# Kernel optimization log

Measured on AMD Instinct MI355X. Metric: run time of the kernel, lower is better.

## Reference

```python
import jax, jax.numpy as jnp
import numpy as np

HIDDEN = 2048
NUM_HEADS = 16
HEAD_DIM = HIDDEN // NUM_HEADS
HARMONICS = 64


def _holo_params(key, in_features, out_features, harmonics):
    kb, kp = jax.random.split(key)
    basis = jax.random.normal(kb, (harmonics, in_features), dtype=jnp.float32)
    basis = basis / jnp.linalg.norm(basis, axis=1, keepdims=True)  # F.normalize(p=2, dim=1)
    phase = jax.random.normal(kp, (out_features, harmonics), dtype=jnp.float32) * 0.1
    amp = jnp.ones((out_features, harmonics), dtype=jnp.float32) / np.sqrt(harmonics).astype(np.float32)
    return basis, phase, amp


def setup_inputs() -> dict:
    key = jax.random.key(0)
    ks = jax.random.split(key, 5)
    hidden_states = jax.random.normal(ks[0], (2, 2048, HIDDEN), dtype=jnp.float32)
    inp = {"hidden_states": hidden_states}
    for name, k in zip(("q", "k", "v", "o"), ks[1:]):
        basis, phase, amp = _holo_params(k, HIDDEN, HIDDEN, HARMONICS)
        inp[f"basis_{name}"] = basis
        inp[f"phase_{name}"] = phase
        inp[f"amp_{name}"] = amp
    return inp


def _holo_linear(x, basis, phase, amp):
    # resonance: (B,S,H) = x @ basis^T; modulated-sum == resonance @ (amp*cos(phase))^T
    resonance = jnp.einsum('bsd,hd->bsh', x, basis)
    w = amp * jnp.cos(phase)  # (out, harmonics)
    return jnp.einsum('bsh,oh->bso', resonance, w)


def reference(hidden_states, basis_q, phase_q, amp_q, basis_k, phase_k, amp_k,
              basis_v, phase_v, amp_v, basis_o, phase_o, amp_o):
    bsz, seq_len, _ = hidden_states.shape
    q = _holo_linear(hidden_states, basis_q, phase_q, amp_q)
    k = _holo_linear(hidden_states, basis_k, phase_k, amp_k)
    v = _holo_linear(hidden_states, basis_v, phase_v, amp_v)
    # (B, H, S, Dh)
    q = q.reshape(bsz, seq_len, NUM_HEADS, HEAD_DIM).transpose(0, 2, 1, 3)
    k = k.reshape(bsz, seq_len, NUM_HEADS, HEAD_DIM).transpose(0, 2, 1, 3)
    v = v.reshape(bsz, seq_len, NUM_HEADS, HEAD_DIM).transpose(0, 2, 1, 3)
    scale = 1.0 / np.sqrt(HEAD_DIM).astype(np.float32)
    scores = jnp.einsum('bhqd,bhkd->bhqk', q, k) * scale
    attn = jax.nn.softmax(scores, axis=-1)
    out = jnp.einsum('bhqk,bhkd->bhqd', attn, v)
    out = out.transpose(0, 2, 1, 3).reshape(bsz, seq_len, HIDDEN)
    return _holo_linear(out, basis_o, phase_o, amp_o)
```

## Files before the change

kernel.cpp:

```cpp
#include <hip/hip_runtime.h>
#include <hip/hip_bf16.h>
#include <math.h>

#define HIDDEN 2048
#define HARM   64
#define NHEADS 16
#define HDIM   128
#define SEQ    2048
#define BATCH  2
#define ROWS   (BATCH*SEQ)
#define RN     (ROWS*HARM)
#define PN     ((size_t)ROWS*HIDDEN)

using bf16x8 = __attribute__((ext_vector_type(8))) short;
using f32x16 = __attribute__((ext_vector_type(16))) float;

#if defined(__has_builtin)
#if __has_builtin(__builtin_amdgcn_exp2f)
#define EXP2F(x) __builtin_amdgcn_exp2f(x)
#else
#define EXP2F(x) exp2f(x)
#endif
#else
#define EXP2F(x) exp2f(x)
#endif

__device__ inline void split_bf(float a, ushort& hi, ushort& lo) {
  __hip_bfloat16 h = __float2bfloat16(a);
  float hf = __bfloat162float(h);
  __hip_bfloat16 l = __float2bfloat16(a - hf);
  union { __hip_bfloat16 b; ushort u; } c1, c2;
  c1.b = h; c2.b = l;
  hi = c1.u; lo = c2.u;
}

__global__ __launch_bounds__(256) void prep(
    const float* __restrict__ X,
    const float* __restrict__ pq, const float* __restrict__ aq,
    const float* __restrict__ pk, const float* __restrict__ ak,
    const float* __restrict__ pv, const float* __restrict__ av,
    const float* __restrict__ po, const float* __restrict__ ao,
    const float* __restrict__ bq, const float* __restrict__ bk,
    const float* __restrict__ bv, const float* __restrict__ bo,
    ushort* __restrict__ Xh, ushort* __restrict__ Xl,
    ushort* __restrict__ Wh, ushort* __restrict__ Wl,
    ushort* __restrict__ Bh, ushort* __restrict__ Bl) {
  const int bid = blockIdx.x;
  const int t = threadIdx.x;
  if (bid < 8192) {
    size_t i = ((size_t)bid * 256 + t) * 4;
    float4 v = *(const float4*)&X[i];
    ushort4 h, l;
    split_bf(v.x, h.x, l.x); split_bf(v.y, h.y, l.y);
    split_bf(v.z, h.z, l.z); split_bf(v.w, h.w, l.w);
    *(ushort4*)&Xh[i] = h;
    *(ushort4*)&Xl[i] = l;
  } else if (bid < 10240) {
    int i = (bid - 8192) * 256 + t;
    const int N = HIDDEN * HARM;
    int set = i / N, j = i - set * N;
    const float* p = (set == 0) ? pq : (set == 1) ? pk : (set == 2) ? pv : po;
    const float* a = (set == 0) ? aq : (set == 1) ? ak : (set == 2) ? av : ao;
    float wv = a[j] * cosf(p[j]);
    ushort h, l;
    split_bf(wv, h, l);
    size_t o = (size_t)set * N + j;
    Wh[o] = h; Wl[o] = l;
  } else {
    int idx = bid - 10240;
    int z = idx >> 7, xb = idx & 127;
    const float* S = (z == 0) ? bq : (z == 1) ? bk : (z == 2) ? bv : bo;
    size_t i = ((size_t)xb * 256 + t) * 4;
    float4 v = *(const float4*)&S[i];
    ushort4 h, l;
    split_bf(v.x, h.x, l.x); split_bf(v.y, h.y, l.y);
    split_bf(v.z, h.z, l.z); split_bf(v.w, h.w, l.w);
    size_t o = (size_t)z * HARM * HIDDEN + i;
    *(ushort4*)&Bh[o] = h;
    *(ushort4*)&Bl[o] = l;
  }
}

__global__ __launch_bounds__(256) void gemm_res(
    const ushort* __restrict__ Xh, const ushort* __restrict__ Xl,
    const ushort* __restrict__ Bh, const ushort* __restrict__ Bl,
    float* __restrict__ R0, float* __restrict__ R1, float* __restrict__ R2) {
  const int z = blockIdx.z;
  const ushort* Bhz = Bh + (size_t)z * HARM * HIDDEN;
  const ushort* Blz = Bl + (size_t)z * HARM * HIDDEN;
  float* Rp = (z == 0) ? R0 : (z == 1) ? R1 : R2;
  const int row0 = blockIdx.x * 64;
  const int kc = blockIdx.y;
  __shared__ __align__(16) ushort Xs[2][64][72];
  __shared__ __align__(16) ushort Bs[2][64][72];
  const int t = threadIdx.x;
  const int lane = t & 63, w = t >> 6;
  const int l31 = lane & 31, hh = lane >> 5;
  const int m0 = (w & 1) * 32, n0 = (w >> 1) * 32;
  const int srow = t >> 2;
  const int sc = (t & 3) * 16;
  f32x16 acc;
  #pragma unroll
  for (int j = 0; j < 16; ++j) acc[j] = 0.0f;

  const int kbase = kc * 512;
  for (int k0 = kbase; k0 < kbase + 512; k0 += 64) {
    const size_t xo = (size_t)(row0 + srow) * HIDDEN + k0 + sc;
    const size_t bo = (size_t)srow * HIDDEN + k0 + sc;
    *(uint4*)&Xs[0][srow][sc]     = *(const uint4*)&Xh[xo];
    *(uint4*)&Xs[0][srow][sc + 8] = *(const uint4*)&Xh[xo + 8];
    *(uint4*)&Xs[1][srow][sc]     = *(const uint4*)&Xl[xo];
    *(uint4*)&Xs[1][srow][sc + 8] = *(const uint4*)&Xl[xo + 8];
    *(uint4*)&Bs[0][srow][sc]     = *(const uint4*)&Bhz[bo];
    *(uint4*)&Bs[0][srow][sc + 8] = *(const uint4*)&Bhz[bo + 8];
    *(uint4*)&Bs[1][srow][sc]     = *(const uint4*)&Blz[bo];
    *(uint4*)&Bs[1][srow][sc + 8] = *(const uint4*)&Blz[bo + 8];
    __syncthreads();
    #pragma unroll
    for (int ks = 0; ks < 4; ++ks) {
      bf16x8 ah = *(const bf16x8*)&Xs[0][m0 + l31][ks * 16 + 8 * hh];
      bf16x8 al = *(const bf16x8*)&Xs[1][m0 + l31][ks * 16 + 8 * hh];
      bf16x8 bh = *(const bf16x8*)&Bs[0][n0 + l31][ks * 16 + 8 * hh];
      bf16x8 bl = *(const bf16x8*)&Bs[1][n0 + l31][ks * 16 + 8 * hh];
      acc = __builtin_amdgcn_mfma_f32_32x32x16_bf16(ah, bh, acc, 0, 0, 0);
      acc = __builtin_amdgcn_mfma_f32_32x32x16_bf16(al, bh, acc, 0, 0, 0);
      acc = __builtin_amdgcn_mfma_f32_32x32x16_bf16(ah, bl, acc, 0, 0, 0);
    }
    __syncthreads();
  }
  float* out = Rp + (size_t)kc * ROWS * HARM;
  #pragma unroll
  for (int r = 0; r < 16; ++r) {
    int mloc = (r & 3) + 8 * (r >> 2) + 4 * hh;
    out[(size_t)(row0 + m0 + mloc) * HARM + n0 + l31] = acc[r];
  }
}

__global__ __launch_bounds__(256) void gemm_proj(
    const float* __restrict__ Rp0, const float* __restrict__ Rp1,
    const float* __restrict__ Rp2,
    const ushort* __restrict__ Wh, const ushort* __restrict__ Wl,
    ushort* __restrict__ P0, ushort* __restrict__ P1, ushort* __restrict__ Vt) {
  const int z = blockIdx.z;
  const float* Rp = (z == 0) ? Rp0 : (z == 1) ? Rp1 : Rp2;
  const ushort* Whz = Wh + (size_t)z * HIDDEN * HARM;
  const ushort* Wlz = Wl + (size_t)z * HIDDEN * HARM;
  const int row0 = blockIdx.x * 32;
  const int col0 = blockIdx.y * 128;
  __shared__ __align__(16) union PSM {
    struct { ushort Rs[2][32][72]; ushort Ws[2][128][72]; } s;
    ushort ct[128][36];
  } sm;
  const int t = threadIdx.x;
  const int lane = t & 63, w = t >> 6;
  const int l31 = lane & 31, hh = lane >> 5;
  {
    const int r = t >> 3, h0 = (t & 7) * 8;
    const size_t o = (size_t)(row0 + r) * HARM + h0;
    #pragma unroll
    for (int e = 0; e < 8; ++e) {
      float v = Rp[o + e] + Rp[RN + o + e] + Rp[2 * (size_t)RN + o + e] +
                Rp[3 * (size_t)RN + o + e];
      ushort hi, lo;
      split_bf(v, hi, lo);
      sm.s.Rs[0][r][h0 + e] = hi;
      sm.s.Rs[1][r][h0 + e] = lo;
    }
  }
  #pragma unroll
  for (int i = 0; i < 4; ++i) {
    int idx = t + i * 256;
    int o = idx >> 3, c8 = (idx & 7) * 8;
    const size_t go = (size_t)(col0 + o) * HARM + c8;
    *(uint4*)&sm.s.Ws[0][o][c8] = *(const uint4*)&Whz[go];
    *(uint4*)&sm.s.Ws[1][o][c8] = *(const uint4*)&Wlz[go];
  }
  __syncthreads();
  const int n0 = w * 32;
  f32x16 acc;
  #pragma unroll
  for (int j = 0; j < 16; ++j) acc[j] = 0.0f;
  #pragma unroll
  for (int ks = 0; ks < 4; ++ks) {
    bf16x8 ah = *(const bf16x8*)&sm.s.Rs[0][l31][ks * 16 + 8 * hh];
    bf16x8 al = *(const bf16x8*)&sm.s.Rs[1][l31][ks * 16 + 8 * hh];
    bf16x8 bh = *(const bf16x8*)&sm.s.Ws[0][n0 + l31][ks * 16 + 8 * hh];
    bf16x8 bl = *(const bf16x8*)&sm.s.Ws[1][n0 + l31][ks * 16 + 8 * hh];
    acc = __builtin_amdgcn_mfma_f32_32x32x16_bf16(ah, bh, acc, 0, 0, 0);
    acc = __builtin_amdgcn_mfma_f32_32x32x16_bf16(al, bh, acc, 0, 0, 0);
    acc = __builtin_amdgcn_mfma_f32_32x32x16_bf16(ah, bl, acc, 0, 0, 0);
  }
  if (z < 2) {
    ushort* P = (z == 0) ? P0 : P1;
    #pragma unroll
    for (int r = 0; r < 16; ++r) {
      int mloc = (r & 3) + 8 * (r >> 2) + 4 * hh;
      union { __hip_bfloat16 b; ushort u; } cv;
      cv.b = __float2bfloat16(acc[r]);
      P[(size_t)(row0 + mloc) * HIDDEN + col0 + n0 + l31] = cv.u;
    }
  } else {
    __syncthreads();
    #pragma unroll
    for (int r = 0; r < 16; ++r) {
      int mloc = (r & 3) + 8 * (r >> 2) + 4 * hh;
      union { __hip_bfloat16 b; ushort u; } cv;
      cv.b = __float2bfloat16(acc[r]);
      sm.ct[n0 + l31][mloc] = cv.u;
    }
    __syncthreads();
    if (t < 128) {
      const int batch = row0 >> 11;
      const int tok0 = row0 & 2047;
      ushort* dst = Vt + (size_t)batch * SEQ * HIDDEN +
                    (size_t)(col0 + t) * SEQ + tok0;
      #pragma unroll
      for (int j = 0; j < 4; ++j)
        *(uint4*)&dst[j * 8] = *(const uint4*)&sm.ct[t][j * 8];
    }
  }
}

__global__ __launch_bounds__(256) void gemm_proj_f32(
    const float* __restrict__ Rp,
    const ushort* __restrict__ Whz, const ushort* __restrict__ Wlz,
    float* __restrict__ P) {
  const int row0 = blockIdx.x * 32;
  const int col0 = blockIdx.y * 128;
  __shared__ __align__(16) ushort Rs[2][32][72];
  __shared__ __align__(16) ushort Ws[2][128][72];
  const int t = threadIdx.x;
  const int lane = t & 63, w = t >> 6;
  const int l31 = lane & 31, hh = lane >> 5;
  {
    const int r = t >> 3, h0 = (t & 7) * 8;
    const size_t o = (size_t)(row0 + r) * HARM + h0;
    #pragma unroll
    for (int e = 0; e < 8; ++e) {
      float v = Rp[o + e] + Rp[RN + o + e] + Rp[2 * (size_t)RN + o + e] +
                Rp[3 * (size_t)RN + o + e];
      ushort hi, lo;
      split_bf(v, hi, lo);
      Rs[0][r][h0 + e] = hi;
      Rs[1][r][h0 + e] = lo;
    }
  }
  #pragma unroll
  for (int i = 0; i < 4; ++i) {
    int idx = t + i * 256;
    int o = idx >> 3, c8 = (idx & 7) * 8;
    const size_t go = (size_t)(col0 + o) * HARM + c8;
    *(uint4*)&Ws[0][o][c8] = *(const uint4*)&Whz[go];
    *(uint4*)&Ws[1][o][c8] = *(const uint4*)&Wlz[go];
  }
  __syncthreads();
  const int n0 = w * 32;
  f32x16 acc;
  #pragma unroll
  for (int j = 0; j < 16; ++j) acc[j] = 0.0f;
  #pragma unroll
  for (int ks = 0; ks < 4; ++ks) {
    bf16x8 ah = *(const bf16x8*)&Rs[0][l31][ks * 16 + 8 * hh];
    bf16x8 al = *(const bf16x8*)&Rs[1][l31][ks * 16 + 8 * hh];
    bf16x8 bh = *(const bf16x8*)&Ws[0][n0 + l31][ks * 16 + 8 * hh];
    bf16x8 bl = *(const bf16x8*)&Ws[1][n0 + l31][ks * 16 + 8 * hh];
    acc = __builtin_amdgcn_mfma_f32_32x32x16_bf16(ah, bh, acc, 0, 0, 0);
    acc = __builtin_amdgcn_mfma_f32_32x32x16_bf16(al, bh, acc, 0, 0, 0);
    acc = __builtin_amdgcn_mfma_f32_32x32x16_bf16(ah, bl, acc, 0, 0, 0);
  }
  #pragma unroll
  for (int r = 0; r < 16; ++r) {
    int mloc = (r & 3) + 8 * (r >> 2) + 4 * hh;
    P[(size_t)(row0 + mloc) * HIDDEN + col0 + n0 + l31] = acc[r];
  }
}

#define BQ 128
#define BK 64
#define KSTR 136
#define VSTR 72

__device__ inline unsigned pkbf(float a, float b) {
  __hip_bfloat162 h2 = __float22bfloat162_rn(make_float2(a, b));
  union { __hip_bfloat162 h; unsigned u; } cv; cv.h = h2; return cv.u;
}

__global__ __launch_bounds__(256, 2) void attn_mfma(
    const ushort* __restrict__ Qg, const ushort* __restrict__ Kg,
    const ushort* __restrict__ Vt, ushort* __restrict__ Oh,
    ushort* __restrict__ Ol) {
  __shared__ __align__(16) union SM {
    ushort q[BQ][KSTR];
    struct { ushort k[BK][KSTR]; ushort v[HDIM][VSTR]; } kv[2];
  } sm;
  const int t = threadIdx.x;
  const int bh = blockIdx.x & 31;
  const int qt = blockIdx.x >> 5;
  const int b = bh >> 4, h = bh & 15;
  const int q0 = qt * BQ;
  const int lane = t & 63;
  const int w = t >> 6;
  const int l31 = lane & 31;
  const int hh = lane >> 5;
  const bool hi = (hh != 0);
  const float SC2 = 0.08838834764831845f * 1.4426950408889634f;

  const int sk_key = t >> 4;
  const int sk_d0 = (t & 15) * 8;
  const int sv_d = t >> 3;
  const int sv_k = (t & 7) * 8;
  const size_t kbase = ((size_t)(b * SEQ)) * HIDDEN + h * HDIM;
  const size_t vbase = ((size_t)(b * SEQ + h * HDIM)) * SEQ;

  {
    const size_t gbase = ((size_t)(b * SEQ + q0)) * HIDDEN + h * HDIM;
    for (int p = 0; p < 8; ++p) {
      int row = p * 16 + sk_key;
      uint4 v = *(const uint4*)&Qg[gbase + (size_t)row * HIDDEN + sk_d0];
      *(uint4*)&sm.q[row][sk_d0] = v;
    }
  }
  __syncthreads();
  bf16x8 Qf[8];
  {
    const int qrow = w * 32 + l31;
    #pragma unroll
    for (int ks = 0; ks < 8; ++ks)
      Qf[ks] = *(const bf16x8*)&sm.q[qrow][ks * 16 + 8 * hh];
  }
  __syncthreads();

  float mrow = -1e30f, lsum = 0.0f;
  f32x16 Ot[4];
  #pragma unroll
  for (int i = 0; i < 4; ++i)
    #pragma unroll
    for (int j = 0; j < 16; ++j) Ot[i][j] = 0.0f;
  f32x16 Zv;
  #pragma unroll
  for (int j = 0; j < 16; ++j) Zv[j] = 0.0f;

  uint4 kp[4], vp[4];
  {
    const size_t gb = kbase;
    #pragma unroll
    for (int p = 0; p < 4; ++p)
      kp[p] = *(const uint4*)&Kg[gb + (size_t)(p * 16 + sk_key) * HIDDEN + sk_d0];
    #pragma unroll
    for (int p = 0; p < 4; ++p)
      vp[p] = *(const uint4*)&Vt[vbase + (size_t)(p * 32 + sv_d) * SEQ + sv_k];
    #pragma unroll
    for (int p = 0; p < 4; ++p)
      *(uint4*)&sm.kv[0].k[p * 16 + sk_key][sk_d0] = kp[p];
    #pragma unroll
    for (int p = 0; p < 4; ++p)
      *(uint4*)&sm.kv[0].v[p * 32 + sv_d][sv_k] = vp[p];
  }
  __syncthreads();

  for (int ci = 0; ci < 32; ++ci) {
    {
      const int cn = (ci < 31) ? ci + 1 : 31;
      const size_t gb = kbase + (size_t)(cn * BK) * HIDDEN;
      #pragma unroll
      for (int p = 0; p < 4; ++p)
        kp[p] = *(const uint4*)&Kg[gb + (size_t)(p * 16 + sk_key) * HIDDEN + sk_d0];
      const size_t vb = vbase + cn * BK;
      #pragma unroll
      for (int p = 0; p < 4; ++p)
        vp[p] = *(const uint4*)&Vt[vb + (size_t)(p * 32 + sv_d) * SEQ + sv_k];
    }
    const int cb = ci & 1;

    f32x16 C0, C1;
    {
      bf16x8 a0 = *(const bf16x8*)&sm.kv[cb].k[l31][8 * hh];
      bf16x8 a1 = *(const bf16x8*)&sm.kv[cb].k[32 + l31][8 * hh];
      __builtin_amdgcn_s_setprio(1);
      C0 = __builtin_amdgcn_mfma_f32_32x32x16_bf16(a0, Qf[0], Zv, 0, 0, 0);
      C1 = __builtin_amdgcn_mfma_f32_32x32x16_bf16(a1, Qf[0], Zv, 0, 0, 0);
      #pragma unroll
      for (int ks = 1; ks < 8; ++ks) {
        bf16x8 b0 = *(const bf16x8*)&sm.kv[cb].k[l31][ks * 16 + 8 * hh];
        bf16x8 b1 = *(const bf16x8*)&sm.kv[cb].k[32 + l31][ks * 16 + 8 * hh];
        C0 = __builtin_amdgcn_mfma_f32_32x32x16_bf16(b0, Qf[ks], C0, 0, 0, 0);
        C1 = __builtin_amdgcn_mfma_f32_32x32x16_bf16(b1, Qf[ks], C1, 0, 0, 0);
      }
      __builtin_amdgcn_s_setprio(0);
    }

    float m01[16];
    #pragma unroll
    for (int j = 0; j < 16; ++j) m01[j] = fmaxf(C0[j], C1[j]);
    float x0 = fmaxf(fmaxf(m01[0], m01[1]), m01[2]);
    float x1 = fmaxf(fmaxf(m01[3], m01[4]), m01[5]);
    float x2 = fmaxf(fmaxf(m01[6], m01[7]), m01[8]);
    float x3 = fmaxf(fmaxf(m01[9], m01[10]), m01[11]);
    float x4 = fmaxf(fmaxf(m01[12], m01[13]), m01[14]);
    float mxr = fmaxf(fmaxf(fmaxf(x0, x1), fmaxf(x2, x3)), fmaxf(x4, m01[15]));
    mxr = fmaxf(mxr, __shfl_xor(mxr, 32));

    const float mg = mxr * SC2;
    if (__any(mg > mrow)) {
      const float mnew = fmaxf(mrow, mg);
      const float alpha = EXP2F(mrow - mnew);
      lsum *= alpha;
      #pragma unroll
      for (int i = 0; i < 4; ++i)
        #pragma unroll
        for (int j = 0; j < 16; ++j) Ot[i][j] *= alpha;
      mrow = mnew;
    }
    float s0 = 0.0f, s1 = 0.0f, s2 = 0.0f, s3 = 0.0f;
    #pragma unroll
    for (int j = 0; j < 16; ++j) {
      float e0 = EXP2F(fmaf(C0[j], SC2, -mrow));
      float e1 = EXP2F(fmaf(C1[j], SC2, -mrow));
      C0[j] = e0; C1[j] = e1;
      if (j & 1) { s2 += e0; s3 += e1; } else { s0 += e0; s1 += e1; }
    }
    lsum += (s0 + s1) + (s2 + s3);

    #pragma unroll
    for (int st = 0; st < 4; ++st) {
      const int eb = 8 * (st & 1);
      float o0, o1, o2, o3, g0, g1, g2, g3;
      if (st < 2) {
        o0 = hi ? C0[eb + 4] : C0[eb + 0]; o1 = hi ? C0[eb + 5] : C0[eb + 1];
        o2 = hi ? C0[eb + 6] : C0[eb + 2]; o3 = hi ? C0[eb + 7] : C0[eb + 3];
        g0 = hi ? C0[eb + 0] : C0[eb + 4]; g1 = hi ? C0[eb + 1] : C0[eb + 5];
        g2 = hi ? C0[eb + 2] : C0[eb + 6]; g3 = hi ? C0[eb + 3] : C0[eb + 7];
      } else {
        o0 = hi ? C1[eb + 4] : C1[eb + 0]; o1 = hi ? C1[eb + 5] : C1[eb + 1];
        o2 = hi ? C1[eb + 6] : C1[eb + 2]; o3 = hi ? C1[eb + 7] : C1[eb + 3];
        g0 = hi ? C1[eb + 0] : C1[eb + 4]; g1 = hi ? C1[eb + 1] : C1[eb + 5];
        g2 = hi ? C1[eb + 2] : C1[eb + 6]; g3 = hi ? C1[eb + 3] : C1[eb + 7];
      }
      unsigned so0 = pkbf(o0, o1), so1 = pkbf(o2, o3);
      unsigned sp0 = pkbf(g0, g1), sp1 = pkbf(g2, g3);
      unsigned r0 = (unsigned)__shfl_xor((int)sp0, 32);
      unsigned r1 = (unsigned)__shfl_xor((int)sp1, 32);
      union { unsigned u[4]; bf16x8 v; } cv;
      cv.u[0] = hi ? r0 : so0;
      cv.u[1] = hi ? r1 : so1;
      cv.u[2] = hi ? so0 : r0;
      cv.u[3] = hi ? so1 : r1;
      __builtin_amdgcn_s_setprio(1);
      #pragma unroll
      for (int mt = 0; mt < 4; ++mt) {
        bf16x8 a2 = *(const bf16x8*)&sm.kv[cb].v[mt * 32 + l31][st * 16 + 8 * hh];
        Ot[mt] = __builtin_amdgcn_mfma_f32_32x32x16_bf16(a2, cv.v, Ot[mt], 0, 0, 0);
      }
      __builtin_amdgcn_s_setprio(0);
    }

    {
      const int nb = cb ^ 1;
      #pragma unroll
      for (int p = 0; p < 4; ++p)
        *(uint4*)&sm.kv[nb].k[p * 16 + sk_key][sk_d0] = kp[p];
      #pragma unroll
      for (int p = 0; p < 4; ++p)
        *(uint4*)&sm.kv[nb].v[p * 32 + sv_d][sv_k] = vp[p];
    }
    __syncthreads();
  }

  lsum += __shfl_xor(lsum, 32);
  const float inv = 1.0f / lsum;
  const int qrow = q0 + w * 32 + l31;
  const size_t ob = ((size_t)(b * SEQ + qrow)) * HIDDEN + h * HDIM;
  #pragma unroll
  for (int mt = 0; mt < 4; ++mt)
    #pragma unroll
    for (int g = 0; g < 4; ++g) {
      ushort4 hs, ls;
      split_bf(Ot[mt][4 * g + 0] * inv, hs.x, ls.x);
      split_bf(Ot[mt][4 * g + 1] * inv, hs.y, ls.y);
      split_bf(Ot[mt][4 * g + 2] * inv, hs.z, ls.z);
      split_bf(Ot[mt][4 * g + 3] * inv, hs.w, ls.w);
      const size_t off = ob + mt * 32 + 8 * g + 4 * hh;
      *(ushort4*)&Oh[off] = hs;
      *(ushort4*)&Ol[off] = ls;
    }
}

extern "C" void kernel_launch(void* const* d_in, const int* in_sizes, int n_in,
                              void* d_out, int out_size, void* d_ws, size_t ws_size,
                              hipStream_t stream) {
  (void)in_sizes; (void)n_in; (void)out_size; (void)ws_size;
  const float* X       = (const float*)d_in[0];
  const float* basis_q = (const float*)d_in[1];
  const float* phase_q = (const float*)d_in[2];
  const float* amp_q   = (const float*)d_in[3];
  const float* basis_k = (const float*)d_in[4];
  const float* phase_k = (const float*)d_in[5];
  const float* amp_k   = (const float*)d_in[6];
  const float* basis_v = (const float*)d_in[7];
  const float* phase_v = (const float*)d_in[8];
  const float* amp_v   = (const float*)d_in[9];
  const float* basis_o = (const float*)d_in[10];
  const float* phase_o = (const float*)d_in[11];
  const float* amp_o   = (const float*)d_in[12];

  const size_t WN = (size_t)HIDDEN * HARM;

  char* p = (char*)d_ws;
  ushort* Xhi = (ushort*)p; p += PN * 2;
  ushort* Xlo = (ushort*)p; p += PN * 2;
  ushort* Bhi = (ushort*)p; p += 4 * WN * 2;
  ushort* Blo = (ushort*)p; p += 4 * WN * 2;
  ushort* Whi = (ushort*)p; p += 4 * WN * 2;
  ushort* Wlo = (ushort*)p; p += 4 * WN * 2;
  float* Rqp = (float*)p; p += (size_t)4 * RN * 4;
  float* Rkp = (float*)p; p += (size_t)4 * RN * 4;
  float* Rvp = (float*)p; p += (size_t)4 * RN * 4;
  float* Rop = (float*)p; p += (size_t)4 * RN * 4;
  __hip_bfloat16* Qb = (__hip_bfloat16*)p; p += PN * 2;
  __hip_bfloat16* Kb = (__hip_bfloat16*)p; p += PN * 2;
  __hip_bfloat16* VtB = (__hip_bfloat16*)p; p += PN * 2;
  ushort* AOh = (ushort*)p; p += PN * 2;
  ushort* AOl = (ushort*)p; p += PN * 2;
  float* out = (float*)d_out;

  prep<<<10752, 256, 0, stream>>>(X,
                                  phase_q, amp_q, phase_k, amp_k,
                                  phase_v, amp_v, phase_o, amp_o,
                                  basis_q, basis_k, basis_v, basis_o,
                                  Xhi, Xlo, Whi, Wlo, Bhi, Blo);

  gemm_res<<<dim3(64, 4, 3), 256, 0, stream>>>(Xhi, Xlo, Bhi, Blo, Rqp, Rkp, Rvp);

  gemm_proj<<<dim3(128, 16, 3), 256, 0, stream>>>(
      Rqp, Rkp, Rvp, Whi, Wlo, (ushort*)Qb, (ushort*)Kb, (ushort*)VtB);

  attn_mfma<<<dim3((SEQ / BQ) * 32), 256, 0, stream>>>(
      (const ushort*)Qb, (const ushort*)Kb, (const ushort*)VtB, AOh, AOl);

  gemm_res<<<dim3(64, 4, 1), 256, 0, stream>>>(
      AOh, AOl, Bhi + 3 * WN, Blo + 3 * WN, Rop, Rop, Rop);

  gemm_proj_f32<<<dim3(128, 16), 256, 0, stream>>>(
      Rop, Whi + 3 * WN, Wlo + 3 * WN, out);
}
```

Baseline: 257.0 us.

## Fuse Q/K/V resonance GEMMs into one block sharing X tiles; use permlane32 swap

```diff
diff --git a/kernel.cpp b/kernel.cpp
--- a/kernel.cpp
+++ b/kernel.cpp
@@ -14,6 +14,7 @@
 
 using bf16x8 = __attribute__((ext_vector_type(8))) short;
 using f32x16 = __attribute__((ext_vector_type(16))) float;
+using u32x2  = __attribute__((ext_vector_type(2))) unsigned;
 
 #if defined(__has_builtin)
 #if __has_builtin(__builtin_amdgcn_exp2f)
@@ -23,6 +24,37 @@
 #endif
 #else
 #define EXP2F(x) exp2f(x)
+#endif
+
+#if defined(__has_builtin) && __has_builtin(__builtin_amdgcn_permlane32_swap)
+__device__ inline void plane_swap_u(unsigned& a, unsigned& b) {
+  u32x2 r = __builtin_amdgcn_permlane32_swap(a, b, false, false);
+  a = r[0]; b = r[1];
+}
+__device__ inline void plane_swap_f(float& a, float& b) {
+  union { float f; unsigned u; } ua, ub;
+  ua.f = a; ub.f = b;
+  u32x2 r = __builtin_amdgcn_permlane32_swap(ua.u, ub.u, false, false);
+  ua.u = r[0]; ub.u = r[1];
+  a = ua.f; b = ub.f;
+}
+#else
+__device__ inline void plane_swap_u(unsigned& a, unsigned& b) {
+  const bool hi = (threadIdx.x & 32) != 0;
+  unsigned ax = (unsigned)__shfl_xor((int)a, 32);
+  unsigned bx = (unsigned)__shfl_xor((int)b, 32);
+  unsigned r0 = hi ? bx : a;
+  unsigned r1 = hi ? b : ax;
+  a = r0; b = r1;
+}
+__device__ inline void plane_swap_f(float& a, float& b) {
+  const bool hi = (threadIdx.x & 32) != 0;
+  float ax = __shfl_xor(a, 32);
+  float bx = __shfl_xor(b, 32);
+  float r0 = hi ? bx : a;
+  float r1 = hi ? b : ax;
+  a = r0; b = r1;
+}
 #endif
 
 __device__ inline void split_bf(float a, ushort& hi, ushort& lo) {
@@ -81,6 +113,66 @@
   }
 }
 
+__global__ __launch_bounds__(768) void gemm_res3(
+    const ushort* __restrict__ Xh, const ushort* __restrict__ Xl,
+    const ushort* __restrict__ Bh, const ushort* __restrict__ Bl,
+    float* __restrict__ R0, float* __restrict__ R1, float* __restrict__ R2) {
+  const int row0 = blockIdx.x * 64;
+  const int kc = blockIdx.y;
+  __shared__ __align__(16) ushort Xs[2][64][72];
+  __shared__ __align__(16) ushort Bs[3][2][64][72];
+  const int t = threadIdx.x;
+  const int lane = t & 63, w = t >> 6;
+  const int l31 = lane & 31, hh = lane >> 5;
+  const int z = w >> 2;
+  const int wq = w & 3;
+  const int m0 = (wq & 1) * 32, n0 = (wq >> 1) * 32;
+  f32x16 acc;
+  #pragma unroll
+  for (int j = 0; j < 16; ++j) acc[j] = 0.0f;
+
+  const int kbase = kc * 512;
+  for (int k0 = kbase; k0 < kbase + 512; k0 += 64) {
+    #pragma unroll
+    for (int it = 0; it < 6; ++it) {
+      int idx = t + it * 768;
+      if (idx < 4096) {
+        int s = idx >> 9, r = (idx >> 3) & 63, c8 = (idx & 7) * 8;
+        if (s < 2) {
+          const ushort* src = s ? Xl : Xh;
+          *(uint4*)&Xs[s][r][c8] =
+              *(const uint4*)&src[(size_t)(row0 + r) * HIDDEN + k0 + c8];
+        } else {
+          int zz = (s - 2) >> 1, pl = (s - 2) & 1;
+          const ushort* src = pl ? Bl : Bh;
+          *(uint4*)&Bs[zz][pl][r][c8] =
+              *(const uint4*)&src[(size_t)zz * HARM * HIDDEN +
+                                  (size_t)r * HIDDEN + k0 + c8];
+        }
+      }
+    }
+    __syncthreads();
+    #pragma unroll
+    for (int ks = 0; ks < 4; ++ks) {
+      bf16x8 ah = *(const bf16x8*)&Xs[0][m0 + l31][ks * 16 + 8 * hh];
+      bf16x8 al = *(const bf16x8*)&Xs[1][m0 + l31][ks * 16 + 8 * hh];
+      bf16x8 bh = *(const bf16x8*)&Bs[z][0][n0 + l31][ks * 16 + 8 * hh];
+      bf16x8 bl = *(const bf16x8*)&Bs[z][1][n0 + l31][ks * 16 + 8 * hh];
+      acc = __builtin_amdgcn_mfma_f32_32x32x16_bf16(ah, bh, acc, 0, 0, 0);
+      acc = __builtin_amdgcn_mfma_f32_32x32x16_bf16(al, bh, acc, 0, 0, 0);
+      acc = __builtin_amdgcn_mfma_f32_32x32x16_bf16(ah, bl, acc, 0, 0, 0);
+    }
+    __syncthreads();
+  }
+  float* Rp = (z == 0) ? R0 : (z == 1) ? R1 : R2;
+  float* out = Rp + (size_t)kc * ROWS * HARM;
+  #pragma unroll
+  for (int r = 0; r < 16; ++r) {
+    int mloc = (r & 3) + 8 * (r >> 2) + 4 * hh;
+    out[(size_t)(row0 + m0 + mloc) * HARM + n0 + l31] = acc[r];
+  }
+}
+
 __global__ __launch_bounds__(256) void gemm_res(
     const ushort* __restrict__ Xh, const ushort* __restrict__ Xl,
     const ushort* __restrict__ Bh, const ushort* __restrict__ Bl,
@@ -302,7 +394,6 @@
   const int w = t >> 6;
   const int l31 = lane & 31;
   const int hh = lane >> 5;
-  const bool hi = (hh != 0);
   const float SC2 = 0.08838834764831845f * 1.4426950408889634f;
 
   const int sk_key = t >> 4;
@@ -398,7 +489,11 @@
     float x3 = fmaxf(fmaxf(m01[9], m01[10]), m01[11]);
     float x4 = fmaxf(fmaxf(m01[12], m01[13]), m01[14]);
     float mxr = fmaxf(fmaxf(fmaxf(x0, x1), fmaxf(x2, x3)), fmaxf(x4, m01[15]));
-    mxr = fmaxf(mxr, __shfl_xor(mxr, 32));
+    {
+      float u = mxr, v2 = mxr;
+      plane_swap_f(u, v2);
+      mxr = fmaxf(u, v2);
+    }
 
     const float mg = mxr * SC2;
     if (__any(mg > mrow)) {
@@ -424,27 +519,18 @@
     #pragma unroll
     for (int st = 0; st < 4; ++st) {
       const int eb = 8 * (st & 1);
-      float o0, o1, o2, o3, g0, g1, g2, g3;
+      unsigned A0, A1, B0, B1;
       if (st < 2) {
-        o0 = hi ? C0[eb + 4] : C0[eb + 0]; o1 = hi ? C0[eb + 5] : C0[eb + 1];
-        o2 = hi ? C0[eb + 6] : C0[eb + 2]; o3 = hi ? C0[eb + 7] : C0[eb + 3];
-        g0 = hi ? C0[eb + 0] : C0[eb + 4]; g1 = hi ? C0[eb + 1] : C0[eb + 5];
-        g2 = hi ? C0[eb + 2] : C0[eb + 6]; g3 = hi ? C0[eb + 3] : C0[eb + 7];
+        A0 = pkbf(C0[eb + 0], C0[eb + 1]); A1 = pkbf(C0[eb + 2], C0[eb + 3]);
+        B0 = pkbf(C0[eb + 4], C0[eb + 5]); B1 = pkbf(C0[eb + 6], C0[eb + 7]);
       } else {
-        o0 = hi ? C1[eb + 4] : C1[eb + 0]; o1 = hi ? C1[eb + 5] : C1[eb + 1];
-        o2 = hi ? C1[eb + 6] : C1[eb + 2]; o3 = hi ? C1[eb + 7] : C1[eb + 3];
-        g0 = hi ? C1[eb + 0] : C1[eb + 4]; g1 = hi ? C1[eb + 1] : C1[eb + 5];
-        g2 = hi ? C1[eb + 2] : C1[eb + 6]; g3 = hi ? C1[eb + 3] : C1[eb + 7];
+        A0 = pkbf(C1[eb + 0], C1[eb + 1]); A1 = pkbf(C1[eb + 2], C1[eb + 3]);
+        B0 = pkbf(C1[eb + 4], C1[eb + 5]); B1 = pkbf(C1[eb + 6], C1[eb + 7]);
       }
-      unsigned so0 = pkbf(o0, o1), so1 = pkbf(o2, o3);
-      unsigned sp0 = pkbf(g0, g1), sp1 = pkbf(g2, g3);
-      unsigned r0 = (unsigned)__shfl_xor((int)sp0, 32);
-      unsigned r1 = (unsigned)__shfl_xor((int)sp1, 32);
+      plane_swap_u(A0, B0);
+      plane_swap_u(A1, B1);
       union { unsigned u[4]; bf16x8 v; } cv;
-      cv.u[0] = hi ? r0 : so0;
-      cv.u[1] = hi ? r1 : so1;
-      cv.u[2] = hi ? so0 : r0;
-      cv.u[3] = hi ? so1 : r1;
+      cv.u[0] = A0; cv.u[1] = A1; cv.u[2] = B0; cv.u[3] = B1;
       __builtin_amdgcn_s_setprio(1);
       #pragma unroll
       for (int mt = 0; mt < 4; ++mt) {
@@ -466,7 +552,11 @@
     __syncthreads();
   }
 
-  lsum += __shfl_xor(lsum, 32);
+  {
+    float u = lsum, v2 = lsum;
+    plane_swap_f(u, v2);
+    lsum = u + v2;
+  }
   const float inv = 1.0f / lsum;
   const int qrow = q0 + w * 32 + l31;
   const size_t ob = ((size_t)(b * SEQ + qrow)) * HIDDEN + h * HDIM;
@@ -529,7 +619,7 @@
                                   basis_q, basis_k, basis_v, basis_o,
                                   Xhi, Xlo, Whi, Wlo, Bhi, Blo);
 
-  gemm_res<<<dim3(64, 4, 3), 256, 0, stream>>>(Xhi, Xlo, Bhi, Blo, Rqp, Rkp, Rvp);
+  gemm_res3<<<dim3(64, 4), 768, 0, stream>>>(Xhi, Xlo, Bhi, Blo, Rqp, Rkp, Rvp);
 
   gemm_proj<<<dim3(128, 16, 3), 256, 0, stream>>>(
       Rqp, Rkp, Rvp, Whi, Wlo, (ushort*)Qb, (ushort*)Kb, (ushort*)VtB);
```

After: 268.8 us. 4.6% more time.
